# Kernel optimization log

Measured on AMD Instinct MI355X. Metric: run time of the kernel, lower is better.

The kernel has to match this reference:

```python
import jax, jax.numpy as jnp
import numpy as np

D, F, E, K = 1024, 2048, 8, 2
EPS = 1.1920929e-07  # torch.finfo(float32).eps, RMSNorm default eps=None


def setup_inputs() -> dict:
    key = jax.random.key(0)
    ks = jax.random.split(key, 6)
    x = jax.random.normal(ks[0], (2, 2048, D), jnp.float32)
    Wg = jax.random.normal(ks[1], (D, E), jnp.float32)          # Gate.weights ~ randn
    norm_w = jnp.ones((E, D), jnp.float32)                       # per-expert RMSNorm weight
    W1 = jax.random.normal(ks[2], (E, D, F), jnp.float32) * 0.02
    b1 = jnp.zeros((E, F), jnp.float32)
    W2 = jax.random.normal(ks[3], (E, D, F), jnp.float32) * 0.02
    b2 = jnp.zeros((E, F), jnp.float32)
    W3 = jax.random.normal(ks[4], (E, F, D), jnp.float32) * 0.02
    b3 = jnp.zeros((E, D), jnp.float32)
    return {"x": x, "Wg": Wg, "norm_w": norm_w, "W1": W1, "b1": b1,
            "W2": W2, "b2": b2, "W3": W3, "b3": b3, "k": K}


def reference(x, Wg, norm_w, W1, b1, W2, b2, W3, b3, k):
    orig_shape = x.shape
    xt = x.reshape(-1, x.shape[-1])                    # [T, d]
    num_experts = Wg.shape[-1]

    # --- Gate: top-k then softmax over selected logits ---
    scores = xt @ Wg                                   # [T, E]
    top_v, top_i = jax.lax.top_k(scores, k)            # [T, k]
    gates = jax.nn.softmax(top_v, axis=-1)             # [T, k]
    # combine weight per (token, expert); zero for unrouted experts
    comb = jnp.einsum('tk,tke->te', gates,
                      jax.nn.one_hot(top_i, num_experts, dtype=gates.dtype))  # [T, E]

    # --- Per-expert SwiGLU FFN with RMSNorm (norm weight folded into W1/W2) ---
    inv = jax.lax.rsqrt(jnp.mean(xt * xt, axis=-1, keepdims=True) + EPS)
    xh = xt * inv                                      # [T, d] (un-weighted RMSNorm)
    W1p = norm_w[:, :, None] * W1                      # [E, d, f]
    W2p = norm_w[:, :, None] * W2
    a = jnp.einsum('td,edf->etf', xh, W1p) + b1[:, None, :]   # [E, T, f]
    g = jnp.einsum('td,edf->etf', xh, W2p) + b2[:, None, :]
    h = jax.nn.silu(a) * g                             # [E, T, f]
    o = jnp.einsum('etf,efd->etd', h, W3) + b3[:, None, :]    # [E, T, d]

    # --- Weighted combine (comb==0 for unrouted -> identical to masked loop) ---
    y = jnp.einsum('etd,te->td', o, comb)              # [T, d]
    return y.reshape(orig_shape)
```

## Files before the change

### kernel.cpp

```cpp
#include <hip/hip_runtime.h>
#include <hip/hip_bf16.h>

typedef unsigned short u16;
typedef __attribute__((ext_vector_type(8))) short bf16x8;
typedef __attribute__((ext_vector_type(4))) float f32x4;

#define D_DIM 1024
#define F_DIM 2048
#define E_NUM 8
#define EPS_RMS 1.1920929e-07f
#define NCHUNK 16

__device__ __forceinline__ u16 f2bf(float f) {
  union { float f; unsigned u; } v; v.f = f;
  unsigned r = v.u + 0x7FFFu + ((v.u >> 16) & 1u);
  return (u16)(r >> 16);
}

__device__ __forceinline__ void async16(const void* g, void* l) {
  __builtin_amdgcn_global_load_lds((const __attribute__((address_space(1))) void*)g,
                                   (__attribute__((address_space(3))) void*)l, 16, 0, 0);
}

__global__ __launch_bounds__(256) void gate_kernel(
    const float* __restrict__ x, const float* __restrict__ Wg,
    u16* __restrict__ xh, int* __restrict__ topi, float* __restrict__ gatev)
{
  const int t = blockIdx.x;
  const int tid = threadIdx.x;
  const float4 xv = reinterpret_cast<const float4*>(x + (size_t)t * D_DIM)[tid];
  float ss = xv.x*xv.x + xv.y*xv.y + xv.z*xv.z + xv.w*xv.w;
  float s[8];
#pragma unroll
  for (int e = 0; e < 8; ++e) s[e] = 0.f;
  const float xa[4] = {xv.x, xv.y, xv.z, xv.w};
#pragma unroll
  for (int j = 0; j < 4; ++j) {
    const float4* wr = reinterpret_cast<const float4*>(Wg + (size_t)(tid*4 + j) * 8);
    float4 w0 = wr[0], w1 = wr[1];
    s[0] += xa[j]*w0.x; s[1] += xa[j]*w0.y; s[2] += xa[j]*w0.z; s[3] += xa[j]*w0.w;
    s[4] += xa[j]*w1.x; s[5] += xa[j]*w1.y; s[6] += xa[j]*w1.z; s[7] += xa[j]*w1.w;
  }
#pragma unroll
  for (int off = 32; off > 0; off >>= 1) {
    ss += __shfl_down(ss, off);
#pragma unroll
    for (int e = 0; e < 8; ++e) s[e] += __shfl_down(s[e], off);
  }
  __shared__ float red[4][9];
  __shared__ float invs;
  const int wv = tid >> 6, lane = tid & 63;
  if (lane == 0) { red[wv][8] = ss;
#pragma unroll
    for (int e = 0; e < 8; ++e) red[wv][e] = s[e]; }
  __syncthreads();
  if (tid == 0) {
    float sum2 = red[0][8] + red[1][8] + red[2][8] + red[3][8];
    invs = rsqrtf(sum2 * (1.0f / D_DIM) + EPS_RMS);
    float sc[8];
#pragma unroll
    for (int e = 0; e < 8; ++e) sc[e] = red[0][e] + red[1][e] + red[2][e] + red[3][e];
    int i0 = 0; float v0 = sc[0];
#pragma unroll
    for (int e = 1; e < 8; ++e) if (sc[e] > v0) { v0 = sc[e]; i0 = e; }
    int i1 = -1; float v1 = -3.0e38f;
#pragma unroll
    for (int e = 0; e < 8; ++e) if (e != i0 && sc[e] > v1) { v1 = sc[e]; i1 = e; }
    float p1 = 1.0f / (1.0f + expf(v0 - v1));
    float p0 = 1.0f - p1;
    topi[2*t] = i0; topi[2*t+1] = i1;
    gatev[2*t] = p0; gatev[2*t+1] = p1;
  }
  __syncthreads();
  const float inv = invs;
  ushort4 o;
  o.x = f2bf(xv.x*inv); o.y = f2bf(xv.y*inv); o.z = f2bf(xv.z*inv); o.w = f2bf(xv.w*inv);
  reinterpret_cast<ushort4*>(xh + (size_t)t * D_DIM)[tid] = o;
}

__global__ __launch_bounds__(256) void count_kernel(
    const int* __restrict__ topi, int* __restrict__ percnt, int nent)
{
  const int blk = blockIdx.x;
  const int tid = threadIdx.x;
  const int per = (nent + NCHUNK*256 - 1) / (NCHUNK*256);
  const int cbase = blk * 256 * per;
  int c[8];
#pragma unroll
  for (int q = 0; q < 8; ++q) c[q] = 0;
  for (int i = 0; i < per; ++i) {
    const int idx = cbase + tid * per + i;
    if (idx < nent) {
      const int e = topi[idx];
#pragma unroll
      for (int q = 0; q < 8; ++q) c[q] += (e == q) ? 1 : 0;
    }
  }
#pragma unroll
  for (int off = 32; off > 0; off >>= 1)
#pragma unroll
    for (int q = 0; q < 8; ++q) c[q] += __shfl_down(c[q], off);
  __shared__ int red[4][8];
  const int wv = tid >> 6, lane = tid & 63;
  if (lane == 0)
#pragma unroll
    for (int q = 0; q < 8; ++q) red[wv][q] = c[q];
  __syncthreads();
  if (tid < 8) percnt[blk * 8 + tid] = red[0][tid] + red[1][tid] + red[2][tid] + red[3][tid];
}

__global__ void scan_kernel(const int* __restrict__ percnt, int* __restrict__ offs,
                            int* __restrict__ base)
{
  if (threadIdx.x == 0) {
    int tot[8];
#pragma unroll
    for (int e = 0; e < 8; ++e) {
      tot[e] = 0;
      for (int c = 0; c < NCHUNK; ++c) tot[e] += percnt[c*8 + e];
    }
    int acc = 0, start[8];
#pragma unroll
    for (int e = 0; e < 8; ++e) { offs[e] = acc; start[e] = acc; acc += (tot[e] + 255) & ~255; }
    offs[8] = acc;
    for (int c = 0; c < NCHUNK; ++c)
#pragma unroll
      for (int e = 0; e < 8; ++e) { base[c*8 + e] = start[e]; start[e] += percnt[c*8 + e]; }
  }
}

__global__ __launch_bounds__(256) void scatter_kernel(
    const int* __restrict__ topi, const int* __restrict__ base,
    int* __restrict__ rowtok, int* __restrict__ slots, int nent)
{
  __shared__ int cur[8];
  const int blk = blockIdx.x, tid = threadIdx.x;
  if (tid < 8) cur[tid] = base[blk*8 + tid];
  __syncthreads();
  const int per = (nent + NCHUNK*256 - 1) / (NCHUNK*256);
  const int cbase = blk * 256 * per;
  for (int i = 0; i < per; ++i) {
    const int idx = cbase + tid * per + i;
    if (idx < nent) {
      const int e = topi[idx];
      const int pos = atomicAdd(&cur[e], 1);
      rowtok[pos] = idx >> 1;
      slots[idx] = pos;
    }
  }
}

__global__ __launch_bounds__(256) void transpose_fold_w12(
    const float* __restrict__ W1, const float* __restrict__ W2,
    const float* __restrict__ scale,
    u16* __restrict__ W1t, u16* __restrict__ W2t)
{
  __shared__ float tile[64][65];
  const int z = blockIdx.z;
  const int e = z & 7;
  const float* W = (z < 8) ? W1 : W2;
  u16* out = (z < 8) ? W1t : W2t;
  const int R = D_DIM, C = F_DIM;
  const int cb = blockIdx.x * 64, rb = blockIdx.y * 64;
  const int tx = threadIdx.x;
  const int ty = threadIdx.y;
  const float* Wp = W + (size_t)e * R * C;
#pragma unroll
  for (int rep = 0; rep < 4; ++rep) {
    const int i = ty + rep * 16;
    float4 v = *reinterpret_cast<const float4*>(Wp + (size_t)(rb + i) * C + cb + tx * 4);
    tile[i][tx*4+0] = v.x; tile[i][tx*4+1] = v.y; tile[i][tx*4+2] = v.z; tile[i][tx*4+3] = v.w;
  }
  __syncthreads();
  float sc[4];
#pragma unroll
  for (int q = 0; q < 4; ++q) sc[q] = scale[(size_t)e * R + rb + tx*4 + q];
  u16* op = out + (size_t)e * R * C;
#pragma unroll
  for (int rep = 0; rep < 4; ++rep) {
    const int j = ty + rep * 16;
    ushort4 o;
    o.x = f2bf(tile[tx*4+0][j] * sc[0]);
    o.y = f2bf(tile[tx*4+1][j] * sc[1]);
    o.z = f2bf(tile[tx*4+2][j] * sc[2]);
    o.w = f2bf(tile[tx*4+3][j] * sc[3]);
    *reinterpret_cast<ushort4*>(op + (size_t)(cb + j) * R + rb + tx*4) = o;
  }
}

__global__ __launch_bounds__(256) void transpose_w3(
    const float* __restrict__ W, u16* __restrict__ out)
{
  __shared__ float tile[64][65];
  const int e = blockIdx.z;
  const int R = F_DIM, C = D_DIM;
  const int cb = blockIdx.x * 64, rb = blockIdx.y * 64;
  const int tx = threadIdx.x, ty = threadIdx.y;
  const float* Wp = W + (size_t)e * R * C;
#pragma unroll
  for (int rep = 0; rep < 4; ++rep) {
    const int i = ty + rep * 16;
    float4 v = *reinterpret_cast<const float4*>(Wp + (size_t)(rb + i) * C + cb + tx * 4);
    tile[i][tx*4+0] = v.x; tile[i][tx*4+1] = v.y; tile[i][tx*4+2] = v.z; tile[i][tx*4+3] = v.w;
  }
  __syncthreads();
  u16* op = out + (size_t)e * R * C;
#pragma unroll
  for (int rep = 0; rep < 4; ++rep) {
    const int j = ty + rep * 16;
    ushort4 o;
    o.x = f2bf(tile[tx*4+0][j]);
    o.y = f2bf(tile[tx*4+1][j]);
    o.z = f2bf(tile[tx*4+2][j]);
    o.w = f2bf(tile[tx*4+3][j]);
    *reinterpret_cast<ushort4*>(op + (size_t)(cb + j) * R + rb + tx*4) = o;
  }
}

__global__ __launch_bounds__(512, 2) void ffn1_kernel(
    const u16* __restrict__ xh, const u16* __restrict__ W1t, const u16* __restrict__ W2t,
    const float* __restrict__ b1, const float* __restrict__ b2,
    const int* __restrict__ rowtok, const int* __restrict__ offs,
    u16* __restrict__ h)
{
  __shared__ __align__(16) u16 smem[65536];

  const int row0 = blockIdx.y * 256;
  if (row0 >= offs[8]) return;
  int e = 0;
#pragma unroll
  for (int i = 1; i < 8; ++i) e += (row0 >= offs[i]) ? 1 : 0;

  const int n0 = blockIdx.x * 128;
  const int tid = threadIdx.x;
  const int lane = tid & 63;
  const int wv = tid >> 6;
  const int wm = wv >> 1;
  const int wn = wv & 1;

  const int srow = tid >> 3;
  const int sseg = (tid & 7) ^ (srow & 7);
  int tokA[4];
#pragma unroll
  for (int j = 0; j < 4; ++j) {
    int tk = rowtok[row0 + srow + 64*j];
    tokA[j] = (tk < 0) ? 0 : tk;
  }
  const u16* gA[4];
#pragma unroll
  for (int j = 0; j < 4; ++j) gA[j] = xh + (size_t)tokA[j] * D_DIM + sseg * 8;
  const u16* gB1[2]; const u16* gB2[2];
#pragma unroll
  for (int j = 0; j < 2; ++j) {
    const size_t wrow = (size_t)e * F_DIM + n0 + srow + 64*j;
    gB1[j] = W1t + wrow * D_DIM + sseg * 8;
    gB2[j] = W2t + wrow * D_DIM + sseg * 8;
  }

  const f32x4 zero = {0.f, 0.f, 0.f, 0.f};
  f32x4 acc1[4][4], acc2[4][4];
#pragma unroll
  for (int i = 0; i < 4; ++i)
#pragma unroll
    for (int j = 0; j < 4; ++j) { acc1[i][j] = zero; acc2[i][j] = zero; }

  const int rswz = (lane & 7) << 3;
  const int kpart = (lane >> 4) * 8;
  const int arowbase = (wm*64 + (lane & 15)) * 64;
  const int browbase = (wn*64 + (lane & 15)) * 64;

#define STAGE(b, k0)                                                        \
  {                                                                         \
    const int aB = (b)*16384, b1B = 32768 + (b)*8192, b2B = 49152 + (b)*8192; \
    _Pragma("unroll")                                                       \
    for (int j = 0; j < 4; ++j)                                             \
      async16(gA[j] + (k0), &smem[aB + (tid + 512*j)*8]);                   \
    _Pragma("unroll")                                                       \
    for (int j = 0; j < 2; ++j) {                                           \
      async16(gB1[j] + (k0), &smem[b1B + (tid + 512*j)*8]);                 \
      async16(gB2[j] + (k0), &smem[b2B + (tid + 512*j)*8]);                 \
    }                                                                       \
  }

  STAGE(0, 0);
  __syncthreads();

  int cur = 0;
  for (int t = 0; t < D_DIM/64; ++t) {
    if (t + 1 < D_DIM/64) STAGE(cur ^ 1, (t+1)*64);
    const int aB = cur*16384, b1B = 32768 + cur*8192, b2B = 49152 + cur*8192;
#pragma unroll
    for (int kk = 0; kk < 2; ++kk) {
      const int ko = kk*32 + kpart;
      bf16x8 af[4], bv1[4], bv2[4];
#pragma unroll
      for (int mi = 0; mi < 4; ++mi)
        af[mi] = *(const bf16x8*)(&smem[aB + ((arowbase + mi*1024 + ko) ^ rswz)]);
#pragma unroll
      for (int ni = 0; ni < 4; ++ni) {
        bv1[ni] = *(const bf16x8*)(&smem[b1B + ((browbase + ni*1024 + ko) ^ rswz)]);
        bv2[ni] = *(const bf16x8*)(&smem[b2B + ((browbase + ni*1024 + ko) ^ rswz)]);
      }
#pragma unroll
      for (int mi = 0; mi < 4; ++mi)
#pragma unroll
        for (int ni = 0; ni < 4; ++ni) {
          acc1[mi][ni] = __builtin_amdgcn_mfma_f32_16x16x32_bf16(af[mi], bv1[ni], acc1[mi][ni], 0, 0, 0);
          acc2[mi][ni] = __builtin_amdgcn_mfma_f32_16x16x32_bf16(af[mi], bv2[ni], acc2[mi][ni], 0, 0, 0);
        }
    }
    __syncthreads();
    cur ^= 1;
  }
#undef STAGE

#pragma unroll
  for (int mi = 0; mi < 4; ++mi) {
    const int rbase = row0 + wm*64 + mi*16 + (lane >> 4)*4;
#pragma unroll
    for (int ni = 0; ni < 4; ++ni) {
      const int gc = n0 + wn*64 + ni*16 + (lane & 15);
      const float bb1 = b1[e*F_DIM + gc], bb2 = b2[e*F_DIM + gc];
#pragma unroll
      for (int r = 0; r < 4; ++r) {
        float a = acc1[mi][ni][r] + bb1;
        float g = acc2[mi][ni][r] + bb2;
        h[(size_t)(rbase + r) * F_DIM + gc] = f2bf(a / (1.f + __expf(-a)) * g);
      }
    }
  }
}

__global__ __launch_bounds__(512, 4) void ffn2_kernel(
    const u16* __restrict__ h, const u16* __restrict__ W3t,
    const float* __restrict__ b3, const int* __restrict__ offs,
    float* __restrict__ opart)
{
  __shared__ __align__(16) u16 sA[4096];
  __shared__ __align__(16) u16 sB[8192];

  const int row0 = blockIdx.y * 128;
  if (row0 >= offs[8]) return;
  int e = 0;
#pragma unroll
  for (int i = 1; i < 8; ++i) e += (row0 >= offs[i]) ? 1 : 0;

  const int n0 = blockIdx.x * 256;
  const int tid = threadIdx.x;
  const int lane = tid & 63;
  const int wv = tid >> 6;
  const int wm = wv >> 2, wn = wv & 3;

  const u16* gA  = h + (size_t)(row0 + (tid >> 2)) * F_DIM + (tid & 3) * 8;
  const u16* gB0 = W3t + ((size_t)e * D_DIM + n0 + (tid >> 2)) * F_DIM + (tid & 3) * 8;
  const u16* gB1 = W3t + ((size_t)e * D_DIM + n0 + 128 + (tid >> 2)) * F_DIM + (tid & 3) * 8;
  u16* lA  = sA + tid * 8;
  u16* lB0 = sB + tid * 8;
  u16* lB1 = sB + 4096 + tid * 8;

  const f32x4 zero = {0.f, 0.f, 0.f, 0.f};
  f32x4 acc[4][4];
#pragma unroll
  for (int i = 0; i < 4; ++i)
#pragma unroll
    for (int j = 0; j < 4; ++j) acc[i][j] = zero;

  const int arow = (lane & 15) * 32 + (lane >> 4) * 8;

  for (int k0 = 0; k0 < F_DIM; k0 += 32) {
    __syncthreads();
    async16(gA + k0, lA);
    async16(gB0 + k0, lB0);
    async16(gB1 + k0, lB1);
    __syncthreads();
    bf16x8 af[4];
#pragma unroll
    for (int mi = 0; mi < 4; ++mi)
      af[mi] = *(const bf16x8*)(sA + (wm*64 + mi*16)*32 + arow);
#pragma unroll
    for (int ni = 0; ni < 4; ++ni) {
      const bf16x8 bv = *(const bf16x8*)(sB + (wn*64 + ni*16)*32 + arow);
#pragma unroll
      for (int mi = 0; mi < 4; ++mi)
        acc[mi][ni] = __builtin_amdgcn_mfma_f32_16x16x32_bf16(af[mi], bv, acc[mi][ni], 0, 0, 0);
    }
  }

#pragma unroll
  for (int mi = 0; mi < 4; ++mi) {
    const int rbase = row0 + wm*64 + mi*16 + (lane >> 4)*4;
#pragma unroll
    for (int ni = 0; ni < 4; ++ni) {
      const int gc = n0 + wn*64 + ni*16 + (lane & 15);
      const float bb = b3[e*D_DIM + gc];
#pragma unroll
      for (int r = 0; r < 4; ++r)
        opart[(size_t)(rbase + r) * D_DIM + gc] = acc[mi][ni][r] + bb;
    }
  }
}

__global__ __launch_bounds__(256) void combine_kernel(
    const float* __restrict__ opart, const int* __restrict__ slots,
    const float* __restrict__ gatev, float* __restrict__ y)
{
  const int t = blockIdx.x;
  const int s0 = slots[2*t], s1 = slots[2*t+1];
  const float w0 = gatev[2*t], w1 = gatev[2*t+1];
  const float4 a = reinterpret_cast<const float4*>(opart + (size_t)s0 * D_DIM)[threadIdx.x];
  const float4 b = reinterpret_cast<const float4*>(opart + (size_t)s1 * D_DIM)[threadIdx.x];
  float4 o;
  o.x = w0*a.x + w1*b.x; o.y = w0*a.y + w1*b.y;
  o.z = w0*a.z + w1*b.z; o.w = w0*a.w + w1*b.w;
  reinterpret_cast<float4*>(y + (size_t)t * D_DIM)[threadIdx.x] = o;
}

extern "C" void kernel_launch(void* const* d_in, const int* in_sizes, int n_in,
                              void* d_out, int out_size, void* d_ws, size_t ws_size,
                              hipStream_t stream)
{
  const float* x  = (const float*)d_in[0];
  const float* Wg = (const float*)d_in[1];
  const float* nw = (const float*)d_in[2];
  const float* W1 = (const float*)d_in[3];
  const float* b1 = (const float*)d_in[4];
  const float* W2 = (const float*)d_in[5];
  const float* b2 = (const float*)d_in[6];
  const float* W3 = (const float*)d_in[7];
  const float* b3 = (const float*)d_in[8];
  float* y = (float*)d_out;

  const int T = in_sizes[0] / D_DIM;
  const int NENT = T * 2;
  const int RCAP = ((NENT + E_NUM * 255) + 255) & ~255;
  const int MT1 = RCAP / 256;
  const int MT2 = RCAP / 128;

  char* ws = (char*)d_ws;
  size_t off_ = 0;
  auto take = [&](size_t bytes) { char* p = ws + off_; off_ = (off_ + bytes + 255) & ~(size_t)255; return p; };
  u16* W1t    = (u16*)take((size_t)E_NUM * F_DIM * D_DIM * 2);
  u16* W2t    = (u16*)take((size_t)E_NUM * F_DIM * D_DIM * 2);
  u16* W3t    = (u16*)take((size_t)E_NUM * D_DIM * F_DIM * 2);
  u16* xh     = (u16*)take((size_t)T * D_DIM * 2);
  u16* hbuf   = (u16*)take((size_t)RCAP * F_DIM * 2);
  int* rowtok = (int*)take((size_t)RCAP * 4);
  int* slots  = (int*)take((size_t)NENT * 4);
  int* topi   = (int*)take((size_t)NENT * 4);
  float* gatev= (float*)take((size_t)NENT * 4);
  int* percnt = (int*)take(NCHUNK * 8 * 4);
  int* cbase  = (int*)take(NCHUNK * 8 * 4);
  int* offs   = (int*)take(64);
  float* opart = (float*)W1t;
  (void)ws_size; (void)n_in; (void)out_size;

  hipMemsetAsync(rowtok, 0xFF, (size_t)RCAP * 4, stream);

  transpose_fold_w12<<<dim3(F_DIM/64, D_DIM/64, 2*E_NUM), dim3(16, 16), 0, stream>>>(W1, W2, nw, W1t, W2t);
  transpose_w3<<<dim3(D_DIM/64, F_DIM/64, E_NUM), dim3(16, 16), 0, stream>>>(W3, W3t);

  gate_kernel<<<T, 256, 0, stream>>>(x, Wg, xh, topi, gatev);
  count_kernel<<<NCHUNK, 256, 0, stream>>>(topi, percnt, NENT);
  scan_kernel<<<1, 64, 0, stream>>>(percnt, offs, cbase);
  scatter_kernel<<<NCHUNK, 256, 0, stream>>>(topi, cbase, rowtok, slots, NENT);

  ffn1_kernel<<<dim3(F_DIM/128, MT1), 512, 0, stream>>>(xh, W1t, W2t, b1, b2, rowtok, offs, hbuf);
  ffn2_kernel<<<dim3(D_DIM/256, MT2), 512, 0, stream>>>(hbuf, W3t, b3, offs, opart);
  combine_kernel<<<T, 256, 0, stream>>>(opart, slots, gatev, y);
}
```

Baseline: 255.0 us.

## Double-buffer ffn2 with 64-wide K stages, swizzled LDS, and MFMA priority

ffn2 is restructured to a 128x128 tile with 256 threads. It double-buffers 64-wide K slices in swizzled LDS, so the next slice loads asynchronously while MFMAs run, and it needs one barrier per iteration instead of two. s_setprio is raised around the MFMA blocks in both ffn1 and ffn2 to favour issuing matrix instructions. The change gives more LDS per block and a different grid shape in exchange for less load stall and fewer bank conflicts.

```diff
diff --git a/kernel.cpp b/kernel.cpp
--- a/kernel.cpp
+++ b/kernel.cpp
@@ -301,6 +301,7 @@
         bv1[ni] = *(const bf16x8*)(&smem[b1B + ((browbase + ni*1024 + ko) ^ rswz)]);
         bv2[ni] = *(const bf16x8*)(&smem[b2B + ((browbase + ni*1024 + ko) ^ rswz)]);
       }
+      __builtin_amdgcn_s_setprio(1);
 #pragma unroll
       for (int mi = 0; mi < 4; ++mi)
 #pragma unroll
@@ -308,6 +309,7 @@
           acc1[mi][ni] = __builtin_amdgcn_mfma_f32_16x16x32_bf16(af[mi], bv1[ni], acc1[mi][ni], 0, 0, 0);
           acc2[mi][ni] = __builtin_amdgcn_mfma_f32_16x16x32_bf16(af[mi], bv2[ni], acc2[mi][ni], 0, 0, 0);
         }
+      __builtin_amdgcn_s_setprio(0);
     }
     __syncthreads();
     cur ^= 1;
@@ -331,13 +333,12 @@
   }
 }
 
-__global__ __launch_bounds__(512, 4) void ffn2_kernel(
+__global__ __launch_bounds__(256, 2) void ffn2_kernel(
     const u16* __restrict__ h, const u16* __restrict__ W3t,
     const float* __restrict__ b3, const int* __restrict__ offs,
     float* __restrict__ opart)
 {
-  __shared__ __align__(16) u16 sA[4096];
-  __shared__ __align__(16) u16 sB[8192];
+  __shared__ __align__(16) u16 smem[32768];
 
   const int row0 = blockIdx.y * 128;
   if (row0 >= offs[8]) return;
@@ -345,18 +346,21 @@
 #pragma unroll
   for (int i = 1; i < 8; ++i) e += (row0 >= offs[i]) ? 1 : 0;
 
-  const int n0 = blockIdx.x * 256;
+  const int n0 = blockIdx.x * 128;
   const int tid = threadIdx.x;
   const int lane = tid & 63;
   const int wv = tid >> 6;
-  const int wm = wv >> 2, wn = wv & 3;
-
-  const u16* gA  = h + (size_t)(row0 + (tid >> 2)) * F_DIM + (tid & 3) * 8;
-  const u16* gB0 = W3t + ((size_t)e * D_DIM + n0 + (tid >> 2)) * F_DIM + (tid & 3) * 8;
-  const u16* gB1 = W3t + ((size_t)e * D_DIM + n0 + 128 + (tid >> 2)) * F_DIM + (tid & 3) * 8;
-  u16* lA  = sA + tid * 8;
-  u16* lB0 = sB + tid * 8;
-  u16* lB1 = sB + 4096 + tid * 8;
+  const int wm = wv >> 1;
+  const int wn = wv & 1;
+
+  const int srow = tid >> 3;
+  const int sseg = (tid & 7) ^ (srow & 7);
+  const u16* gA[4]; const u16* gB[4];
+#pragma unroll
+  for (int j = 0; j < 4; ++j) {
+    gA[j] = h   + (size_t)(row0 + srow + 32*j) * F_DIM + sseg * 8;
+    gB[j] = W3t + ((size_t)e * D_DIM + n0 + srow + 32*j) * F_DIM + sseg * 8;
+  }
 
   const f32x4 zero = {0.f, 0.f, 0.f, 0.f};
   f32x4 acc[4][4];
@@ -365,26 +369,50 @@
 #pragma unroll
     for (int j = 0; j < 4; ++j) acc[i][j] = zero;
 
-  const int arow = (lane & 15) * 32 + (lane >> 4) * 8;
-
-  for (int k0 = 0; k0 < F_DIM; k0 += 32) {
+  const int rswz = (lane & 7) << 3;
+  const int kpart = (lane >> 4) * 8;
+  const int arowbase = (wm*64 + (lane & 15)) * 64;
+  const int browbase = (wn*64 + (lane & 15)) * 64;
+
+#define STAGE2(b, k0)                                                       \
+  {                                                                         \
+    const int aB = (b)*8192, bB = 16384 + (b)*8192;                         \
+    _Pragma("unroll")                                                       \
+    for (int j = 0; j < 4; ++j) {                                           \
+      async16(gA[j] + (k0), &smem[aB + (tid + 256*j)*8]);                   \
+      async16(gB[j] + (k0), &smem[bB + (tid + 256*j)*8]);                   \
+    }                                                                       \
+  }
+
+  STAGE2(0, 0);
+  __syncthreads();
+
+  int cur = 0;
+  for (int t = 0; t < F_DIM/64; ++t) {
+    if (t + 1 < F_DIM/64) STAGE2(cur ^ 1, (t+1)*64);
+    const int aB = cur*8192, bB = 16384 + cur*8192;
+#pragma unroll
+    for (int kk = 0; kk < 2; ++kk) {
+      const int ko = kk*32 + kpart;
+      bf16x8 af[4], bv[4];
+#pragma unroll
+      for (int mi = 0; mi < 4; ++mi)
+        af[mi] = *(const bf16x8*)(&smem[aB + ((arowbase + mi*1024 + ko) ^ rswz)]);
+#pragma unroll
+      for (int ni = 0; ni < 4; ++ni)
+        bv[ni] = *(const bf16x8*)(&smem[bB + ((browbase + ni*1024 + ko) ^ rswz)]);
+      __builtin_amdgcn_s_setprio(1);
+#pragma unroll
+      for (int mi = 0; mi < 4; ++mi)
+#pragma unroll
+        for (int ni = 0; ni < 4; ++ni)
+          acc[mi][ni] = __builtin_amdgcn_mfma_f32_16x16x32_bf16(af[mi], bv[ni], acc[mi][ni], 0, 0, 0);
+      __builtin_amdgcn_s_setprio(0);
+    }
     __syncthreads();
-    async16(gA + k0, lA);
-    async16(gB0 + k0, lB0);
-    async16(gB1 + k0, lB1);
-    __syncthreads();
-    bf16x8 af[4];
-#pragma unroll
-    for (int mi = 0; mi < 4; ++mi)
-      af[mi] = *(const bf16x8*)(sA + (wm*64 + mi*16)*32 + arow);
-#pragma unroll
-    for (int ni = 0; ni < 4; ++ni) {
-      const bf16x8 bv = *(const bf16x8*)(sB + (wn*64 + ni*16)*32 + arow);
-#pragma unroll
-      for (int mi = 0; mi < 4; ++mi)
-        acc[mi][ni] = __builtin_amdgcn_mfma_f32_16x16x32_bf16(af[mi], bv, acc[mi][ni], 0, 0, 0);
-    }
-  }
+    cur ^= 1;
+  }
+#undef STAGE2
 
 #pragma unroll
   for (int mi = 0; mi < 4; ++mi) {
@@ -465,6 +493,6 @@
   scatter_kernel<<<NCHUNK, 256, 0, stream>>>(topi, cbase, rowtok, slots, NENT);
 
   ffn1_kernel<<<dim3(F_DIM/128, MT1), 512, 0, stream>>>(xh, W1t, W2t, b1, b2, rowtok, offs, hbuf);
-  ffn2_kernel<<<dim3(D_DIM/256, MT2), 512, 0, stream>>>(hbuf, W3t, b3, offs, opart);
+  ffn2_kernel<<<dim3(D_DIM/128, MT2), 256, 0, stream>>>(hbuf, W3t, b3, offs, opart);
   combine_kernel<<<T, 256, 0, stream>>>(opart, slots, gatev, y);
 }
```

New measurement: 261.6 us. +2.6%, slower.
